# Optimization experiments

Hardware: AMD Instinct MI355X
Metric: run time of the kernel (lower is better)

Reference implementation:

```python
import jax, jax.numpy as jnp
import numpy as np

P, N, D = 8, 1024, 768
H = 12
HS = D // H
SCALE = float(HS ** 0.5)  # NOTE: original multiplies by sqrt(head_size)


def setup_inputs() -> dict:
    key = jax.random.key(0)
    k1, k2, k3 = jax.random.split(key, 3)
    pixel_values = jax.random.normal(k1, (P, N, D), dtype=jnp.float32)
    attention_mask = jnp.zeros((P, 1, 1, N), dtype=jnp.float32)
    qkv_w = jax.random.normal(k2, (D, 3 * D), dtype=jnp.float32) * 0.02
    qkv_b = jnp.zeros((3 * D,), dtype=jnp.float32)
    proj_w = jax.random.normal(k3, (D, D), dtype=jnp.float32) * 0.02
    proj_b = jnp.zeros((D,), dtype=jnp.float32)
    return {
        "pixel_values": pixel_values,
        "attention_mask": attention_mask,
        "qkv_w": qkv_w,
        "qkv_b": qkv_b,
        "proj_w": proj_w,
        "proj_b": proj_b,
    }


def reference(pixel_values, attention_mask, qkv_w, qkv_b, proj_w, proj_b):
    p, n, d = pixel_values.shape
    # fused QKV projection: (p, n, 3d) -> (3, p, H, n, hs)
    mixed = pixel_values @ qkv_w + qkv_b
    mixed = mixed.reshape(p, n, 3, H, HS).transpose(2, 0, 3, 1, 4)
    q, k, v = mixed[0], mixed[1], mixed[2]
    # scores: (p, H, n, n); original multiplies by sqrt(head_size)
    scores = jnp.einsum("phqd,phkd->phqk", q, k) * SCALE
    probs = jax.nn.softmax(scores, axis=-1)
    # dropout p=0 (identity in eval); mask added POST-softmax, per source
    probs = probs + attention_mask
    ctx = jnp.einsum("phqk,phkd->phqd", probs, v)
    ctx = ctx.transpose(0, 2, 1, 3).reshape(p, n, d)
    out = ctx @ proj_w + proj_b
    return out
```

## Files before the change

kernel.cpp:

```cpp
#include <hip/hip_runtime.h>
#include <hip/hip_bf16.h>
#include <cstdint>
#include <math.h>

constexpr int PB = 8;
constexpr int NS = 1024;
constexpr int DM = 768;
constexpr int NH = 12;
constexpr int HSZ = 64;
constexpr float QS    = 11.541560327111707f;
constexpr float EOFFL = 126.95716359822878f;

typedef short    bf16x8 __attribute__((ext_vector_type(8)));
typedef _Float16 half8  __attribute__((ext_vector_type(8)));
typedef __fp16   fp16x2 __attribute__((ext_vector_type(2)));
typedef float    floatx4 __attribute__((ext_vector_type(4)));

#if __has_builtin(__builtin_amdgcn_exp2f)
#define EXP2(x) __builtin_amdgcn_exp2f(x)
#else
#define EXP2(x) exp2f(x)
#endif

__device__ __forceinline__ ushort f2h(float x) {
    _Float16 h = (_Float16)x;
    return *reinterpret_cast<ushort*>(&h);
}
__device__ __forceinline__ float h2f(ushort u) {
    _Float16 h = __builtin_bit_cast(_Float16, u);
    return (float)h;
}
__device__ __forceinline__ ushort f2bf(float x) {
    __hip_bfloat16 b = __float2bfloat16(x);
    return *reinterpret_cast<ushort*>(&b);
}
__device__ __forceinline__ float bf2f(ushort u) {
    __hip_bfloat16 b = *reinterpret_cast<__hip_bfloat16*>(&u);
    return __bfloat162float(b);
}
__device__ __forceinline__ unsigned int pk2h(float a, float b) {
    fp16x2 h = __builtin_amdgcn_cvt_pkrtz(a, b);
    return __builtin_bit_cast(unsigned int, h);
}

#define GLDS(g, l)                                                             \
    __builtin_amdgcn_global_load_lds(                                          \
        (const __attribute__((address_space(1))) void*)(g),                    \
        (__attribute__((address_space(3))) void*)(l), 16, 0, 0)

__global__ void split_kernel(const float* __restrict__ x, ushort* __restrict__ hf,
                             int n4)
{
    int i = blockIdx.x * blockDim.x + threadIdx.x;
    const int stride = gridDim.x * blockDim.x;
    for (; i < n4; i += stride) {
        const float4 v = ((const float4*)x)[i];
        ((ushort4*)hf)[i] = ushort4{f2h(v.x), f2h(v.y), f2h(v.z), f2h(v.w)};
    }
}

__global__ void splitT_kernel(const float* __restrict__ w, ushort* __restrict__ fT,
                              int K, int N)
{
    __shared__ float tile[32][33];
    const int tx = threadIdx.x, ty = threadIdx.y;
    const int bx = blockIdx.x, by = blockIdx.y;
    #pragma unroll
    for (int r = 0; r < 4; ++r)
        tile[ty + r*8][tx] = w[(size_t)(by*32 + ty + r*8) * N + bx*32 + tx];
    __syncthreads();
    #pragma unroll
    for (int r = 0; r < 4; ++r) {
        const int n = bx*32 + ty + r*8;
        const int k = by*32 + tx;
        fT[(size_t)n * K + k] = f2h(tile[tx][ty + r*8]);
    }
}

template <int MODE>
__global__ __launch_bounds__(256, 3)
void gemm_f16(const ushort* __restrict__ Af, const ushort* __restrict__ Bf,
              const float* __restrict__ bias, float* __restrict__ outf,
              ushort* __restrict__ qf, ushort* __restrict__ kf,
              ushort* __restrict__ vt, int K)
{
    __shared__ __align__(16) ushort As[128*64];
    __shared__ __align__(16) ushort Bs[128*64];

    const int t    = threadIdx.x;
    const int w    = t >> 6;
    const int lane = t & 63;
    const int l15  = lane & 15;
    const int quad = lane >> 4;
    const int wm = w >> 1, wn = w & 1;
    const int m0 = blockIdx.x * 128, n0 = blockIdx.y * 128;

    floatx4 acc[4][4];
    #pragma unroll
    for (int i = 0; i < 4; ++i)
        #pragma unroll
        for (int j = 0; j < 4; ++j) acc[i][j] = floatx4{0.f, 0.f, 0.f, 0.f};

    const int srow8 = lane >> 3;
    const int sslot = lane & 7;

    for (int k0 = 0; k0 < K; k0 += 64) {
        #pragma unroll
        for (int j = 0; j < 4; ++j) {
            const int row = w*32 + j*8 + srow8;
            const int seg = sslot ^ (row & 7);
            const int ldst = (w*32 + j*8) * 64;
            GLDS(Af + (size_t)(m0 + row) * K + k0 + seg*8, As + ldst);
            GLDS(Bf + (size_t)(n0 + row) * K + k0 + seg*8, Bs + ldst);
        }
        __syncthreads();

        #pragma unroll
        for (int h2 = 0; h2 < 2; ++h2) {
            half8 fa[4], fb[4];
            #pragma unroll
            for (int i = 0; i < 4; ++i) {
                const int sl = ((h2*4 + quad) ^ (l15 & 7)) * 8;
                fa[i] = *(const half8*)(As + (wm*64 + i*16 + l15) * 64 + sl);
                fb[i] = *(const half8*)(Bs + (wn*64 + i*16 + l15) * 64 + sl);
            }
            #pragma unroll
            for (int mt = 0; mt < 4; ++mt)
                #pragma unroll
                for (int nt = 0; nt < 4; ++nt)
                    acc[mt][nt] = __builtin_amdgcn_mfma_f32_16x16x32_f16(fa[mt], fb[nt], acc[mt][nt], 0, 0, 0);
        }
        __syncthreads();
    }

    if (MODE == 0) {
        #pragma unroll
        for (int nt = 0; nt < 4; ++nt) {
            const int col = n0 + wn*64 + nt*16 + l15;
            const float bval = bias[col];
            #pragma unroll
            for (int mt = 0; mt < 4; ++mt) {
                const int row0 = m0 + wm*64 + mt*16 + quad*4;
                #pragma unroll
                for (int r = 0; r < 4; ++r)
                    outf[(size_t)(row0 + r) * DM + col] = acc[mt][nt][r] + bval;
            }
        }
    } else {
        const int jbase = n0 + wn*64;
        const int c  = jbase / DM;
        const int hh = (jbase % DM) >> 6;
        const int pp = (m0 + wm*64) >> 10;
        const size_t head = (size_t)pp * NH + hh;
        if (c < 2) {
            ushort* dst = (c == 0 ? qf : kf);
            const float qscale = (c == 0) ? QS : 1.0f;
            #pragma unroll
            for (int nt = 0; nt < 4; ++nt) {
                const int s = nt*16 + l15;
                const float bval = bias[jbase + s];
                #pragma unroll
                for (int mt = 0; mt < 4; ++mt) {
                    const int tok0 = m0 + wm*64 + mt*16 + quad*4;
                    const int nn0  = tok0 & 1023;
                    #pragma unroll
                    for (int r = 0; r < 4; ++r)
                        dst[(head*NS + nn0 + r) * HSZ + s] = f2h((acc[mt][nt][r] + bval) * qscale);
                }
            }
        } else {
            #pragma unroll
            for (int nt = 0; nt < 4; ++nt) {
                const int s = nt*16 + l15;
                const float bval = bias[jbase + s];
                #pragma unroll
                for (int mt = 0; mt < 4; ++mt) {
                    const int tok0 = m0 + wm*64 + mt*16 + quad*4;
                    const int nn0  = tok0 & 1023;
                    ushort4 pk;
                    pk.x = f2bf(acc[mt][nt][0] + bval);
                    pk.y = f2bf(acc[mt][nt][1] + bval);
                    pk.z = f2bf(acc[mt][nt][2] + bval);
                    pk.w = f2bf(acc[mt][nt][3] + bval);
                    *(ushort4*)(vt + (head*HSZ + s) * NS + nn0) = pk;
                }
            }
        }
    }
}

__global__ void mv_kernel(const float* __restrict__ mask, const ushort* __restrict__ vt,
                          float* __restrict__ mv)
{
    __shared__ float red[4][64];
    const int ph = blockIdx.x;
    const int t  = threadIdx.x;
    const int c  = t & 63, part = t >> 6;
    const ushort* vrow = vt + ((size_t)ph * HSZ + c) * NS + part * 256;
    const float*  mrow = mask + (size_t)(ph / NH) * NS + part * 256;
    float acc = 0.f;
    for (int k = 0; k < 256; k += 4) {
        const ushort4 v4 = *(const ushort4*)(vrow + k);
        const float4  m4 = *(const float4*)(mrow + k);
        acc += m4.x * bf2f(v4.x) + m4.y * bf2f(v4.y)
             + m4.z * bf2f(v4.z) + m4.w * bf2f(v4.w);
    }
    red[part][c] = acc;
    __syncthreads();
    if (t < 64)
        mv[(size_t)ph * HSZ + t] = red[0][t] + red[1][t] + red[2][t] + red[3][t];
}

__global__ __launch_bounds__(256, 3)
void attn_mfma_kernel(const ushort* __restrict__ qf, const ushort* __restrict__ kf,
                      const ushort* __restrict__ vt, const float* __restrict__ mv,
                      ushort* __restrict__ ctx)
{
    __shared__ __align__(16) ushort khs[64*64];
    __shared__ __align__(16) ushort vs [64*64];

    const int t    = threadIdx.x;
    const int w    = t >> 6;
    const int lane = t & 63;
    const int l15  = lane & 15;
    const int quad = lane >> 4;
    const int ph = blockIdx.x, qt = blockIdx.y;
    const int h  = ph % NH,    p  = ph / NH;
    const size_t headoff = ((size_t)p * NH + h) * (size_t)(NS * HSZ);

    const ushort* qpa = qf + headoff + (size_t)(qt*128 + w*16 + l15) * HSZ + quad*8;
    const half8 qa0 = *(const half8*)(qpa);
    const half8 qa1 = *(const half8*)(qpa + 32);
    const ushort* qpb = qpa + (size_t)64 * HSZ;
    const half8 qb0 = *(const half8*)(qpb);
    const half8 qb1 = *(const half8*)(qpb + 32);

    floatx4 oA[4], oB[4];
    float lsumA = 0.f, lsumB = 0.f;
    #pragma unroll
    for (int tc = 0; tc < 4; ++tc) {
        oA[tc] = floatx4{0.f, 0.f, 0.f, 0.f};
        oB[tc] = floatx4{0.f, 0.f, 0.f, 0.f};
    }

    const int srow8 = lane >> 3;
    const int sslot = lane & 7;
    const int xs = l15 & 7;

    for (int kt = 0; kt < 16; ++kt) {
        __syncthreads();
        #pragma unroll
        for (int j = 0; j < 2; ++j) {
            const int row  = w*16 + j*8 + srow8;
            const int segK = sslot ^ ((row & 3) | (((row >> 3) & 1) << 2));
            const int segV = sslot ^ (row & 7);
            const size_t gk = headoff + (size_t)(kt*64 + row) * HSZ + segK*8;
            const size_t gv = headoff + (size_t)row * NS + kt*64 + segV*8;
            const int ldst = (w*16 + j*8) * 64;
            GLDS(kf + gk, khs + ldst);
            GLDS(vt + gv, vs  + ldst);
        }
        __syncthreads();

        bf16x8 bpA[2], bpB[2];
        #pragma unroll
        for (int tt = 0; tt < 4; ++tt) {
            const int rho = ((l15 >> 2) << 3) + ((tt & 1) << 2) + (l15 & 3) + ((tt >> 1) << 5);
            const int a0 = rho*64 + ((quad       ^ xs) * 8);
            const int a1 = rho*64 + (((quad | 4) ^ xs) * 8);
            const half8 bh0 = *(const half8*)(khs + a0);
            const half8 bh1 = *(const half8*)(khs + a1);
            floatx4 sA = floatx4{-EOFFL, -EOFFL, -EOFFL, -EOFFL};
            sA = __builtin_amdgcn_mfma_f32_16x16x32_f16(bh0, qa0, sA, 0, 0, 0);
            sA = __builtin_amdgcn_mfma_f32_16x16x32_f16(bh1, qa1, sA, 0, 0, 0);
            floatx4 sB = floatx4{-EOFFL, -EOFFL, -EOFFL, -EOFFL};
            sB = __builtin_amdgcn_mfma_f32_16x16x32_f16(bh0, qb0, sB, 0, 0, 0);
            sB = __builtin_amdgcn_mfma_f32_16x16x32_f16(bh1, qb1, sB, 0, 0, 0);
            const float a0e = EXP2(sA[0]);
            const float a1e = EXP2(sA[1]);
            const float a2e = EXP2(sA[2]);
            const float a3e = EXP2(sA[3]);
            lsumA += (a0e + a1e) + (a2e + a3e);
            const float b0e = EXP2(sB[0]);
            const float b1e = EXP2(sB[1]);
            const float b2e = EXP2(sB[2]);
            const float b3e = EXP2(sB[3]);
            lsumB += (b0e + b1e) + (b2e + b3e);
            const int off = (tt & 1) * 4;
            bf16x8& dA = bpA[tt >> 1];
            dA[off + 0] = (short)f2bf(a0e);
            dA[off + 1] = (short)f2bf(a1e);
            dA[off + 2] = (short)f2bf(a2e);
            dA[off + 3] = (short)f2bf(a3e);
            bf16x8& dB = bpB[tt >> 1];
            dB[off + 0] = (short)f2bf(b0e);
            dB[off + 1] = (short)f2bf(b1e);
            dB[off + 2] = (short)f2bf(b2e);
            dB[off + 3] = (short)f2bf(b3e);
        }

        #pragma unroll
        for (int tc = 0; tc < 4; ++tc) {
            const int crow = (tc*16 + l15) * 64;
            const bf16x8 va0 = *(const bf16x8*)(vs + crow + ((quad       ^ xs) * 8));
            const bf16x8 va1 = *(const bf16x8*)(vs + crow + (((quad | 4) ^ xs) * 8));
            oA[tc] = __builtin_amdgcn_mfma_f32_16x16x32_bf16(va0, bpA[0], oA[tc], 0, 0, 0);
            oA[tc] = __builtin_amdgcn_mfma_f32_16x16x32_bf16(va1, bpA[1], oA[tc], 0, 0, 0);
            oB[tc] = __builtin_amdgcn_mfma_f32_16x16x32_bf16(va0, bpB[0], oB[tc], 0, 0, 0);
            oB[tc] = __builtin_amdgcn_mfma_f32_16x16x32_bf16(va1, bpB[1], oB[tc], 0, 0, 0);
        }
    }

    float lA = lsumA;
    lA += __shfl_xor(lA, 16);
    lA += __shfl_xor(lA, 32);
    const float invA = 1.0f / lA;
    float lB = lsumB;
    lB += __shfl_xor(lB, 16);
    lB += __shfl_xor(lB, 32);
    const float invB = 1.0f / lB;

    const float* mvp = mv + ((size_t)p * NH + h) * HSZ;
    const int rowA = qt*128 + w*16 + l15;
    const size_t baseA = ((size_t)p * NS + rowA) * DM + h * 64;
    const size_t baseB = baseA + (size_t)64 * DM;
    #pragma unroll
    for (int tc = 0; tc < 4; ++tc) {
        const int c0 = tc*16 + quad*4;
        const float m0v = mvp[c0 + 0], m1v = mvp[c0 + 1];
        const float m2v = mvp[c0 + 2], m3v = mvp[c0 + 3];
        uint2 stA;
        stA.x = pk2h(oA[tc][0] * invA + m0v, oA[tc][1] * invA + m1v);
        stA.y = pk2h(oA[tc][2] * invA + m2v, oA[tc][3] * invA + m3v);
        *(uint2*)(ctx + baseA + c0) = stA;
        uint2 stB;
        stB.x = pk2h(oB[tc][0] * invB + m0v, oB[tc][1] * invB + m1v);
        stB.y = pk2h(oB[tc][2] * invB + m2v, oB[tc][3] * invB + m3v);
        *(uint2*)(ctx + baseB + c0) = stB;
    }
}

extern "C" void kernel_launch(void* const* d_in, const int* in_sizes, int n_in,
                              void* d_out, int out_size, void* d_ws, size_t ws_size,
                              hipStream_t stream)
{
    const float* x      = (const float*)d_in[0];
    const float* mask   = (const float*)d_in[1];
    const float* qkv_w  = (const float*)d_in[2];
    const float* qkv_b  = (const float*)d_in[3];
    const float* proj_w = (const float*)d_in[4];
    const float* proj_b = (const float*)d_in[5];
    float* out = (float*)d_out;

    const size_t HE = (size_t)PB * NH * NS * HSZ;
    const size_t QW = (size_t)DM * 3 * DM;
    const size_t PW = (size_t)DM * DM;
    ushort* xf  = (ushort*)d_ws;
    ushort* qwf = xf + HE;
    ushort* pwf = qwf + QW;
    ushort* qfv = pwf + PW;
    ushort* kfv = qfv + HE;
    ushort* vtv = kfv + HE;
    float*  mvb = (float*)(vtv + HE);
    ushort* cth = xf;

    split_kernel<<<2048, 256, 0, stream>>>(x, xf, (int)(HE / 4));
    splitT_kernel<<<dim3(3*DM/32, DM/32), dim3(32, 8), 0, stream>>>(qkv_w, qwf, DM, 3*DM);
    splitT_kernel<<<dim3(DM/32,   DM/32), dim3(32, 8), 0, stream>>>(proj_w, pwf, DM, DM);

    gemm_f16<1><<<dim3(PB*NS/128, 3*DM/128), 256, 0, stream>>>(
        xf, qwf, qkv_b, nullptr, qfv, kfv, vtv, DM);

    mv_kernel<<<dim3(PB*NH), 256, 0, stream>>>(mask, vtv, mvb);

    attn_mfma_kernel<<<dim3(PB*NH, NS/128), 256, 0, stream>>>(
        qfv, kfv, vtv, mvb, cth);

    gemm_f16<0><<<dim3(PB*NS/128, DM/128), 256, 0, stream>>>(
        cth, pwf, proj_b, out, nullptr, nullptr, nullptr, DM);
}
```

Measured before the change: 198.0 us.

## Double-buffer attention K/V LDS tiles and merge preprocessing kernels into one launch

```diff
diff --git a/kernel.cpp b/kernel.cpp
--- a/kernel.cpp
+++ b/kernel.cpp
@@ -48,23 +48,36 @@
         (const __attribute__((address_space(1))) void*)(g),                    \
         (__attribute__((address_space(3))) void*)(l), 16, 0, 0)
 
-__global__ void split_kernel(const float* __restrict__ x, ushort* __restrict__ hf,
-                             int n4)
+__global__ void prep_kernel(const float* __restrict__ x, ushort* __restrict__ hf,
+                            int n4,
+                            const float* __restrict__ qkv_w, ushort* __restrict__ qwf,
+                            const float* __restrict__ proj_w, ushort* __restrict__ pwf)
 {
-    int i = blockIdx.x * blockDim.x + threadIdx.x;
-    const int stride = gridDim.x * blockDim.x;
-    for (; i < n4; i += stride) {
-        const float4 v = ((const float4*)x)[i];
-        ((ushort4*)hf)[i] = ushort4{f2h(v.x), f2h(v.y), f2h(v.z), f2h(v.w)};
-    }
-}
-
-__global__ void splitT_kernel(const float* __restrict__ w, ushort* __restrict__ fT,
-                              int K, int N)
-{
+    const int bid = blockIdx.x;
+    if (bid < 2048) {
+        int i = bid * blockDim.x + threadIdx.x;
+        const int stride = 2048 * blockDim.x;
+        for (; i < n4; i += stride) {
+            const float4 v = ((const float4*)x)[i];
+            ((ushort4*)hf)[i] = ushort4{f2h(v.x), f2h(v.y), f2h(v.z), f2h(v.w)};
+        }
+        return;
+    }
     __shared__ float tile[32][33];
-    const int tx = threadIdx.x, ty = threadIdx.y;
-    const int bx = blockIdx.x, by = blockIdx.y;
+    const int t  = threadIdx.x;
+    const int tx = t & 31, ty = t >> 5;
+    const float* w;
+    ushort* fT;
+    int bx, by, K, N;
+    if (bid < 2048 + 1728) {
+        const int id = bid - 2048;
+        bx = id % 72; by = id / 72;
+        w = qkv_w; fT = qwf; K = DM; N = 3 * DM;
+    } else {
+        const int id = bid - (2048 + 1728);
+        bx = id % 24; by = id / 24;
+        w = proj_w; fT = pwf; K = DM; N = DM;
+    }
     #pragma unroll
     for (int r = 0; r < 4; ++r)
         tile[ty + r*8][tx] = w[(size_t)(by*32 + ty + r*8) * N + bx*32 + tx];
@@ -216,8 +229,8 @@
                       const ushort* __restrict__ vt, const float* __restrict__ mv,
                       ushort* __restrict__ ctx)
 {
-    __shared__ __align__(16) ushort khs[64*64];
-    __shared__ __align__(16) ushort vs [64*64];
+    __shared__ __align__(16) ushort khs[2][64*64];
+    __shared__ __align__(16) ushort vs [2][64*64];
 
     const int t    = threadIdx.x;
     const int w    = t >> 6;
@@ -247,8 +260,7 @@
     const int sslot = lane & 7;
     const int xs = l15 & 7;
 
-    for (int kt = 0; kt < 16; ++kt) {
-        __syncthreads();
+    auto stage = [&](int kt, int b) {
         #pragma unroll
         for (int j = 0; j < 2; ++j) {
             const int row  = w*16 + j*8 + srow8;
@@ -257,10 +269,20 @@
             const size_t gk = headoff + (size_t)(kt*64 + row) * HSZ + segK*8;
             const size_t gv = headoff + (size_t)row * NS + kt*64 + segV*8;
             const int ldst = (w*16 + j*8) * 64;
-            GLDS(kf + gk, khs + ldst);
-            GLDS(vt + gv, vs  + ldst);
-        }
+            GLDS(kf + gk, &khs[b][ldst]);
+            GLDS(vt + gv, &vs [b][ldst]);
+        }
+    };
+
+    stage(0, 0);
+    int cur = 0;
+
+    for (int kt = 0; kt < 16; ++kt) {
         __syncthreads();
+        if (kt + 1 < 16) stage(kt + 1, cur ^ 1);
+
+        const ushort* kbuf = khs[cur];
+        const ushort* vbuf = vs [cur];
 
         bf16x8 bpA[2], bpB[2];
         #pragma unroll
@@ -268,8 +290,8 @@
             const int rho = ((l15 >> 2) << 3) + ((tt & 1) << 2) + (l15 & 3) + ((tt >> 1) << 5);
             const int a0 = rho*64 + ((quad       ^ xs) * 8);
             const int a1 = rho*64 + (((quad | 4) ^ xs) * 8);
-            const half8 bh0 = *(const half8*)(khs + a0);
-            const half8 bh1 = *(const half8*)(khs + a1);
+            const half8 bh0 = *(const half8*)(kbuf + a0);
+            const half8 bh1 = *(const half8*)(kbuf + a1);
             floatx4 sA = floatx4{-EOFFL, -EOFFL, -EOFFL, -EOFFL};
             sA = __builtin_amdgcn_mfma_f32_16x16x32_f16(bh0, qa0, sA, 0, 0, 0);
             sA = __builtin_amdgcn_mfma_f32_16x16x32_f16(bh1, qa1, sA, 0, 0, 0);
@@ -302,13 +324,14 @@
         #pragma unroll
         for (int tc = 0; tc < 4; ++tc) {
             const int crow = (tc*16 + l15) * 64;
-            const bf16x8 va0 = *(const bf16x8*)(vs + crow + ((quad       ^ xs) * 8));
-            const bf16x8 va1 = *(const bf16x8*)(vs + crow + (((quad | 4) ^ xs) * 8));
+            const bf16x8 va0 = *(const bf16x8*)(vbuf + crow + ((quad       ^ xs) * 8));
+            const bf16x8 va1 = *(const bf16x8*)(vbuf + crow + (((quad | 4) ^ xs) * 8));
             oA[tc] = __builtin_amdgcn_mfma_f32_16x16x32_bf16(va0, bpA[0], oA[tc], 0, 0, 0);
             oA[tc] = __builtin_amdgcn_mfma_f32_16x16x32_bf16(va1, bpA[1], oA[tc], 0, 0, 0);
             oB[tc] = __builtin_amdgcn_mfma_f32_16x16x32_bf16(va0, bpB[0], oB[tc], 0, 0, 0);
             oB[tc] = __builtin_amdgcn_mfma_f32_16x16x32_bf16(va1, bpB[1], oB[tc], 0, 0, 0);
         }
+        cur ^= 1;
     }
 
     float lA = lsumA;
@@ -364,9 +387,8 @@
     float*  mvb = (float*)(vtv + HE);
     ushort* cth = xf;
 
-    split_kernel<<<2048, 256, 0, stream>>>(x, xf, (int)(HE / 4));
-    splitT_kernel<<<dim3(3*DM/32, DM/32), dim3(32, 8), 0, stream>>>(qkv_w, qwf, DM, 3*DM);
-    splitT_kernel<<<dim3(DM/32,   DM/32), dim3(32, 8), 0, stream>>>(proj_w, pwf, DM, DM);
+    prep_kernel<<<2048 + 1728 + 576, 256, 0, stream>>>(
+        x, xf, (int)(HE / 4), qkv_w, qwf, proj_w, pwf);
 
     gemm_f16<1><<<dim3(PB*NS/128, 3*DM/128), 256, 0, stream>>>(
         xf, qwf, qkv_b, nullptr, qfv, kfv, vtv, DM);
```

Measured after the change: 190.8 us. 3.6% less time.
